# Optimization experiments

Hardware: AMD Instinct MI355X
Metric: run time of the kernel (lower is better)

The kernel has to match this reference:

```python
import jax, jax.numpy as jnp
import numpy as np

B, T, C, J = 2048, 128, 3, 25   # batch, frames, coords, joints
E = 64                          # structure elements (n_elements)


def setup_inputs() -> dict:
    key = jax.random.key(0)
    k1, k2 = jax.random.split(key)
    x = jax.random.normal(k1, (B, T, C, J), dtype=jnp.float32)
    centres = jax.random.uniform(k2, (E, 2), dtype=jnp.float32)
    sharpness = jnp.full((E, 2), 3.0, dtype=jnp.float32)  # torch init: ones*3
    return {"x": x, "centres": centres, "sharpness": sharpness}


def _mst_deaths(Dm):
    """Prim's MST over dense distance matrix Dm [n,n].
    The multiset of MST edge weights equals the finite death times of the
    0-dim Vietoris-Rips persistence diagram (births are all 0)."""
    n = Dm.shape[0]
    in_tree0 = jnp.zeros(n, dtype=bool).at[0].set(True)

    def step(carry, _):
        mind, in_tree = carry
        masked = jnp.where(in_tree, jnp.inf, mind)  # distance from tree to each node
        j = jnp.argmin(masked)
        w = masked[j]                               # weight of edge added to MST
        in_tree = in_tree.at[j].set(True)
        mind = jnp.minimum(mind, Dm[j])
        return (mind, in_tree), w

    (_, _), deaths = jax.lax.scan(step, (Dm[0], in_tree0), None, length=n - 1)
    return deaths  # [n-1]


def reference(x, centres, sharpness):
    # --- dense preprocessing ---
    h = x.mean(1)                           # [B, C, J]
    h = h[..., :, None] - h[..., None, :]   # [B, C, J, J] pairwise coord diffs
    h = h.mean(-3)                          # [B, J, J]
    h = jnp.sqrt((h * h).sum(axis=1))       # torch.norm(., 2, dim=1) -> [B, J]
    lo, hi = h.min(), h.max()
    rng = hi - lo
    safe = rng > 1e-8
    h = jnp.where(safe, (h - lo) / jnp.where(safe, rng, 1.0), jnp.zeros_like(h))

    # --- Vietoris-Rips dim-0 persistence on point cloud h: B points in J dims ---
    sq = (h * h).sum(-1)
    d2 = sq[:, None] + sq[None, :] - 2.0 * (h @ h.T)       # [B, B]
    Dm = jnp.sqrt(jnp.maximum(d2, 1e-12))
    deaths = _mst_deaths(Dm)                               # [B-1]
    pd = jnp.stack([jnp.zeros_like(deaths), deaths], -1)[None]  # [1, P, 2]

    # --- StructureElementLayer: out[b,e] = sum_p exp(-sum_d s[e,d]^2 (pd-c)^2) ---
    s2 = sharpness * sharpness                             # [E, 2]
    diff = pd[:, :, None, :] - centres[None, None, :, :]   # [1, P, E, 2]
    out = jnp.exp(-(diff * diff * s2).sum(-1)).sum(1)      # [1, E]
    return out
```

## Files before the change

### kernel.cpp

```cpp
#include <hip/hip_runtime.h>
#include <math.h>

#define B_N 2048
#define T_N 128
#define C_N 3
#define J_N 25
#define E_N 64
#define TC  (T_N*C_N)
#define TCJ (TC*J_N)
#define NQ4 (TCJ/4)
#define NC  128

#define D_OFF      0
#define H_OFF      (B_N*B_N)
#define BLO_OFF    (H_OFF + B_N*J_N)
#define BHI_OFF    (BLO_OFF + B_N)
#define DEATHS_OFF (BHI_OFF + B_N)
#define BEST_OFF   (DEATHS_OFF + B_N)
#define COMP_OFF   (BEST_OFF + 4*B_N)
#define GC_OFF     (COMP_OFF + 2*B_N)
#define DC_OFF     (GC_OFF + 2)

typedef unsigned long long u64;
#define U64MAX 0xFFFFFFFFFFFFFFFFull
#define U32INF 0xFFFFFFFFu

__global__ void __launch_bounds__(256) k_reduce(const float* __restrict__ x,
                                                float* __restrict__ ws) {
    __shared__ float4 part[250];
    __shared__ float S[100];
    __shared__ float Mj[25];
    const int t = threadIdx.x, b = blockIdx.x;
    const float4* x4 = (const float4*)(x + (size_t)b * TCJ);
    if (t < 250) {
        float4 a; a.x = a.y = a.z = a.w = 0.f;
        for (int idx = t; idx < NQ4; idx += 250) {
            float4 v = x4[idx];
            a.x += v.x; a.y += v.y; a.z += v.z; a.w += v.w;
        }
        part[t] = a;
    }
    __syncthreads();
    if (t < 25) {
        float4 s = part[t];
        #pragma unroll
        for (int g = 1; g < 10; ++g) {
            float4 v = part[t + 25 * g];
            s.x += v.x; s.y += v.y; s.z += v.z; s.w += v.w;
        }
        S[4*t] = s.x; S[4*t+1] = s.y; S[4*t+2] = s.z; S[4*t+3] = s.w;
    }
    __syncthreads();
    if (t < 25) Mj[t] = (S[t] + S[t+25] + S[t+50] + S[t+75]) * (1.0f / 384.0f);
    __syncthreads();
    if (t < 25) {
        float mj = Mj[t], acc = 0.f;
        #pragma unroll
        for (int i = 0; i < J_N; ++i) { float d = Mj[i] - mj; acc += d * d; }
        float hv = sqrtf(acc);
        ws[H_OFF + b * J_N + t] = hv;
        S[t] = hv;
    }
    __syncthreads();
    if (t == 0) {
        float lo = S[0], hi = S[0];
        #pragma unroll
        for (int i = 1; i < J_N; ++i) { lo = fminf(lo, S[i]); hi = fmaxf(hi, S[i]); }
        ws[BLO_OFF + b] = lo;
        ws[BHI_OFF + b] = hi;
    }
}

__global__ void __launch_bounds__(1024) k_distscan(float* __restrict__ ws) {
    __shared__ float A[16][26];
    __shared__ float Bsh[1024 * J_N];
    const int t = threadIdx.x, blk = blockIdx.x;
    const int ty = t >> 6, tx = t & 63;
    const float* h = ws + H_OFF;
    const int row0 = blk * 16;
    for (int idx = t; idx < 16 * J_N; idx += 1024)
        A[idx / J_N][idx % J_N] = h[(row0 + idx / J_N) * J_N + idx % J_N];
    if (blk < 16) ((unsigned*)(ws + DC_OFF))[blk * 1024 + t] = U32INF;
    if (blk == 0) {
        unsigned* gc = (unsigned*)(ws + COMP_OFF);
        gc[t] = (unsigned)t; gc[t + 1024] = (unsigned)(t + 1024);
        if (t == 0) { ((unsigned*)(ws + GC_OFF))[0] = 0u; ((unsigned*)(ws + GC_OFF))[1] = 0u; }
    }
    const int row = row0 + ty;
    float ar[J_N];
    u64 bestk = U64MAX;
    float* D = ws + D_OFF;
    for (int mt = 0; mt < 2; ++mt) {
        __syncthreads();
        for (int idx = t; idx < 1024 * J_N; idx += 1024)
            Bsh[idx] = h[mt * 1024 * J_N + idx];
        __syncthreads();
        if (mt == 0) {
            #pragma unroll
            for (int k = 0; k < J_N; ++k) ar[k] = A[ty][k];
        }
        #pragma unroll 4
        for (int cc = 0; cc < 16; ++cc) {
            const int col = mt * 1024 + cc * 64 + tx;
            const float* bp = &Bsh[(cc * 64 + tx) * J_N];
            float acc = 0.f;
            #pragma unroll
            for (int k = 0; k < J_N; ++k) { float d = ar[k] - bp[k]; acc += d * d; }
            float dist = sqrtf(fmaxf(acc, 1e-12f));
            D[(size_t)row * B_N + col] = dist;
            if (col != row) {
                unsigned a = min((unsigned)row, (unsigned)col);
                unsigned b2 = max((unsigned)row, (unsigned)col);
                u64 key = ((u64)__float_as_uint(dist) << 32) | (a << 11) | b2;
                if (key < bestk) bestk = key;
            }
        }
    }
    #pragma unroll
    for (int off = 32; off; off >>= 1) {
        u64 o = __shfl_down(bestk, off);
        if (o < bestk) bestk = o;
    }
    if (tx == 0) ((u64*)(ws + BEST_OFF))[row] = bestk;
}

__global__ void __launch_bounds__(1024) k_round(float* __restrict__ ws, int par_in) {
    unsigned* gcnt = (unsigned*)(ws + GC_OFF);
    const unsigned base = gcnt[par_in];
    if (base >= B_N - 1) return;
    __shared__ __align__(16) unsigned comp[B_N];
    __shared__ u64 cb[B_N];
    __shared__ unsigned par[B_N];
    __shared__ unsigned cnt_s;
    const int t = threadIdx.x, blk = blockIdx.x;
    const unsigned* gcomp_in = (const unsigned*)(ws + COMP_OFF) + par_in * B_N;
    unsigned* gcomp_out = (unsigned*)(ws + COMP_OFF) + (par_in ^ 1) * B_N;
    const u64* bin = (const u64*)(ws + BEST_OFF) + par_in * B_N;
    u64* bout = (u64*)(ws + BEST_OFF) + (par_in ^ 1) * B_N;
    float* deaths = ws + DEATHS_OFF;

    if (t == 0) cnt_s = 0u;
    comp[t] = gcomp_in[t]; comp[t + 1024] = gcomp_in[t + 1024];
    cb[t] = U64MAX; cb[t + 1024] = U64MAX;
    __syncthreads();
    #pragma unroll
    for (int i = t; i < B_N; i += 1024) {
        u64 bk = bin[i];
        if (bk != U64MAX) atomicMin(&cb[comp[i]], bk);
    }
    __syncthreads();
    #pragma unroll
    for (int c = t; c < B_N; c += 1024) {
        u64 k = cb[c];
        unsigned p = (unsigned)c;
        if (k != U64MAX) {
            unsigned a  = (unsigned)((k >> 11) & 0x7FFu);
            unsigned b2 = (unsigned)(k & 0x7FFu);
            unsigned ca = comp[a], cbv = comp[b2];
            unsigned c2 = (ca == (unsigned)c) ? cbv : ca;
            p = c2;
            if (!(cb[c2] == k && c2 < (unsigned)c)) {
                unsigned li = atomicAdd(&cnt_s, 1u);
                if (blk == 0) deaths[base + li] = __uint_as_float((unsigned)(k >> 32));
            }
        }
        par[c] = p;
    }
    __syncthreads();
    #pragma unroll
    for (int c = t; c < B_N; c += 1024) {
        unsigned p = par[c];
        if (p != (unsigned)c && par[p] == (unsigned)c && (unsigned)c < p) par[c] = (unsigned)c;
    }
    __syncthreads();
    #pragma unroll
    for (int c = t; c < B_N; c += 1024) {
        unsigned r = par[c];
        while (true) { unsigned pr = par[r]; if (pr == r) break; r = pr; }
        par[c] = r;
    }
    __syncthreads();
    #pragma unroll
    for (int i = t; i < B_N; i += 1024) comp[i] = par[comp[i]];
    __syncthreads();
    const unsigned newbase = base + cnt_s;
    if (blk == 0) {
        gcomp_out[t] = comp[t]; gcomp_out[t + 1024] = comp[t + 1024];
        if (t == 0) { gcnt[par_in ^ 1] = newbase; if (newbase >= B_N - 1) gcnt[par_in] = newbase; }
    }
    if (newbase >= B_N - 1) return;

    const int w = t >> 6, lane = t & 63;
    const int row = blk * 16 + w;
    const unsigned ci = comp[row];
    u64 prev = bin[row];
    {
        unsigned pa = (unsigned)((prev >> 11) & 0x7FFu);
        unsigned pb = (unsigned)(prev & 0x7FFu);
        unsigned jo = (pa == (unsigned)row) ? pb : pa;
        if (comp[jo] != ci) {
            if (lane == 0) bout[row] = prev;
            return;
        }
    }
    const float4* row4 = (const float4*)(ws + D_OFF + (size_t)row * B_N);
    const uint4* comp4 = (const uint4*)comp;
    u64 best = U64MAX;
    #pragma unroll
    for (int k = 0; k < 8; ++k) {
        const int q = k * 64 + lane;
        float4 w4 = row4[q];
        uint4  c4 = comp4[q];
        const unsigned j0 = (unsigned)(q * 4);
        float wv[4] = {w4.x, w4.y, w4.z, w4.w};
        unsigned cv[4] = {c4.x, c4.y, c4.z, c4.w};
        #pragma unroll
        for (int m = 0; m < 4; ++m) {
            if (cv[m] != ci) {
                unsigned j = j0 + m;
                unsigned a = min((unsigned)row, j), b2 = max((unsigned)row, j);
                u64 key = ((u64)__float_as_uint(wv[m]) << 32) | (a << 11) | b2;
                if (key < best) best = key;
            }
        }
    }
    #pragma unroll
    for (int off = 32; off; off >>= 1) {
        u64 o = __shfl_down(best, off);
        if (o < best) best = o;
    }
    if (lane == 0) bout[row] = best;
}

__global__ void __launch_bounds__(1024) k_round4c(float* __restrict__ ws) {
    unsigned* gcnt = (unsigned*)(ws + GC_OFF);
    const unsigned base = gcnt[1];
    if (base >= B_N - 1) return;
    __shared__ __align__(16) unsigned comp[B_N];
    __shared__ __align__(16) unsigned ovl[NC*NC];
    __shared__ unsigned cflag[B_N];
    __shared__ unsigned cnt_s, csum[16];
    u64* cb = (u64*)ovl;
    unsigned* par = ovl + 4096;
    const int t = threadIdx.x, blk = blockIdx.x;
    const unsigned* gcomp_in = (const unsigned*)(ws + COMP_OFF) + B_N;
    const u64* bin = (const u64*)(ws + BEST_OFF) + B_N;
    float* deaths = ws + DEATHS_OFF;

    if (t == 0) cnt_s = 0u;
    comp[t] = gcomp_in[t]; comp[t + 1024] = gcomp_in[t + 1024];
    cb[t] = U64MAX; cb[t + 1024] = U64MAX;
    __syncthreads();
    #pragma unroll
    for (int i = t; i < B_N; i += 1024) {
        u64 bk = bin[i];
        if (bk != U64MAX) atomicMin(&cb[comp[i]], bk);
    }
    __syncthreads();
    #pragma unroll
    for (int c = t; c < B_N; c += 1024) {
        u64 k = cb[c];
        unsigned p = (unsigned)c;
        if (k != U64MAX) {
            unsigned a  = (unsigned)((k >> 11) & 0x7FFu);
            unsigned b2 = (unsigned)(k & 0x7FFu);
            unsigned ca = comp[a], cbv = comp[b2];
            unsigned c2 = (ca == (unsigned)c) ? cbv : ca;
            p = c2;
            if (!(cb[c2] == k && c2 < (unsigned)c)) {
                unsigned li = atomicAdd(&cnt_s, 1u);
                if (blk == 0) deaths[base + li] = __uint_as_float((unsigned)(k >> 32));
            }
        }
        par[c] = p;
    }
    __syncthreads();
    #pragma unroll
    for (int c = t; c < B_N; c += 1024) {
        unsigned p = par[c];
        if (p != (unsigned)c && par[p] == (unsigned)c && (unsigned)c < p) par[c] = (unsigned)c;
    }
    __syncthreads();
    #pragma unroll
    for (int c = t; c < B_N; c += 1024) {
        unsigned r = par[c];
        while (true) { unsigned pr = par[r]; if (pr == r) break; r = pr; }
        par[c] = r;
    }
    __syncthreads();
    #pragma unroll
    for (int i = t; i < B_N; i += 1024) comp[i] = par[comp[i]];
    __syncthreads();
    const unsigned newbase = base + cnt_s;
    if (blk == 0 && t == 0) { gcnt[0] = newbase; gcnt[1] = newbase; }
    if (newbase >= B_N - 1) return;

    cflag[t] = 0u; cflag[t + 1024] = 0u;
    __syncthreads();
    cflag[comp[t]] = 1u; cflag[comp[t + 1024]] = 1u;
    __syncthreads();
    const unsigned lane = t & 63, w = t >> 6;
    unsigned f0 = cflag[2 * t], f1 = cflag[2 * t + 1];
    unsigned s = f0 + f1, sc = s;
    #pragma unroll
    for (int off = 1; off < 64; off <<= 1) {
        unsigned v = __shfl_up(sc, off);
        if (lane >= (unsigned)off) sc += v;
    }
    if (lane == 63) csum[w] = sc;
    __syncthreads();
    if (t < 16) {
        unsigned v = csum[t], acc = v;
        #pragma unroll
        for (int off = 1; off < 16; off <<= 1) {
            unsigned u2 = __shfl_up(acc, off);
            if (t >= off) acc += u2;
        }
        csum[t] = acc - v;
    }
    __syncthreads();
    unsigned off0 = csum[w] + (sc - s);
    __syncthreads();
    if (f0) cflag[2 * t] = off0;
    if (f1) cflag[2 * t + 1] = off0 + f0;
    __syncthreads();

    #pragma unroll
    for (int i = 0; i < 16; ++i) ovl[i * 1024 + t] = U32INF;
    __syncthreads();
    {
        const int row = blk * 16 + (int)w;
        const unsigned ci = comp[row];
        const unsigned ri = cflag[ci];
        const float4* row4 = (const float4*)(ws + D_OFF + (size_t)row * B_N);
        const uint4* comp4 = (const uint4*)comp;
        #pragma unroll
        for (int k = 0; k < 8; ++k) {
            const int q = k * 64 + (int)lane;
            float4 w4 = row4[q];
            uint4  c4 = comp4[q];
            float wv[4] = {w4.x, w4.y, w4.z, w4.w};
            unsigned cv[4] = {c4.x, c4.y, c4.z, c4.w};
            #pragma unroll
            for (int m = 0; m < 4; ++m) {
                if (cv[m] != ci) atomicMin(&ovl[ri * NC + cflag[cv[m]]], __float_as_uint(wv[m]));
            }
        }
    }
    __syncthreads();
    unsigned* gDc = (unsigned*)(ws + DC_OFF);
    #pragma unroll
    for (int i = t; i < NC * NC; i += 1024) {
        unsigned v = ovl[i];
        if (v != U32INF) atomicMin(&gDc[i], v);
    }
}

__global__ void __launch_bounds__(1024) k_finishstruct(float* __restrict__ ws,
                                                       const float* __restrict__ centres,
                                                       const float* __restrict__ sharp,
                                                       float* __restrict__ out) {
    __shared__ unsigned Dcs[NC * NC];
    __shared__ u64 cbf[NC];
    __shared__ unsigned parf[NC], ccomp[NC];
    __shared__ unsigned cnt_s, base_s;
    __shared__ float redlo[16], redhi[16];
    const int t = threadIdx.x;
    const int lane = t & 63, w = t >> 6;
    float* deaths = ws + DEATHS_OFF;
    const unsigned base0 = ((const unsigned*)(ws + GC_OFF))[0];

    if (base0 < B_N - 1) {
        const unsigned* gDc = (const unsigned*)(ws + DC_OFF);
        #pragma unroll
        for (int i = 0; i < 16; ++i) Dcs[i * 1024 + t] = gDc[i * 1024 + t];
        if (t < NC) ccomp[t] = (unsigned)t;
        if (t == 0) base_s = base0;
        __syncthreads();
        for (int iter = 0; iter < 7; ++iter) {
            if (t < NC) cbf[t] = U64MAX;
            if (t == 0) cnt_s = 0u;
            __syncthreads();
            #pragma unroll
            for (int q = 0; q < 8; ++q) {
                const int r = w * 8 + q;
                const unsigned cc = ccomp[r];
                u64 key = U64MAX;
                #pragma unroll
                for (int hh = 0; hh < 2; ++hh) {
                    const int c = lane + hh * 64;
                    unsigned wv = Dcs[r * NC + c];
                    if (wv != U32INF && ccomp[c] != cc) {
                        unsigned a = min((unsigned)r, (unsigned)c);
                        unsigned b2 = max((unsigned)r, (unsigned)c);
                        u64 k2 = ((u64)wv << 32) | (a << 7) | b2;
                        if (k2 < key) key = k2;
                    }
                }
                #pragma unroll
                for (int off = 32; off; off >>= 1) {
                    u64 o = __shfl_down(key, off);
                    if (o < key) key = o;
                }
                if (lane == 0 && key != U64MAX) atomicMin(&cbf[cc], key);
            }
            __syncthreads();
            bool add = false; float dw = 0.f;
            if (t < NC) {
                u64 k = cbf[t];
                unsigned p = (unsigned)t;
                if (k != U64MAX) {
                    unsigned a = (unsigned)((k >> 7) & 127u), b2 = (unsigned)(k & 127u);
                    unsigned ca = ccomp[a], cbv = ccomp[b2];
                    unsigned c2 = (ca == (unsigned)t) ? cbv : ca;
                    p = c2;
                    if (!(cbf[c2] == k && c2 < (unsigned)t)) {
                        add = true; dw = __uint_as_float((unsigned)(k >> 32));
                    }
                }
                parf[t] = p;
            }
            __syncthreads();
            if (t < NC) {
                unsigned pp = parf[t];
                if (pp != (unsigned)t && parf[pp] == (unsigned)t && (unsigned)t < pp) parf[t] = (unsigned)t;
            }
            __syncthreads();
            if (t < NC) {
                unsigned r2 = parf[t];
                while (parf[r2] != r2) r2 = parf[r2];
                parf[t] = r2;
            }
            __syncthreads();
            if (t < NC) {
                if (add) { unsigned li = atomicAdd(&cnt_s, 1u); deaths[base_s + li] = dw; }
                ccomp[t] = parf[ccomp[t]];
            }
            __syncthreads();
            if (t == 0) base_s += cnt_s;
            __syncthreads();
            if (base_s >= B_N - 1) break;
        }
        __threadfence_block();
        __syncthreads();
    }

    float lo = INFINITY, hi = -INFINITY;
    #pragma unroll
    for (int i = t; i < B_N; i += 1024) {
        lo = fminf(lo, ws[BLO_OFF + i]);
        hi = fmaxf(hi, ws[BHI_OFF + i]);
    }
    #pragma unroll
    for (int off = 32; off; off >>= 1) {
        lo = fminf(lo, __shfl_down(lo, off));
        hi = fmaxf(hi, __shfl_down(hi, off));
    }
    if (lane == 0) { redlo[w] = lo; redhi[w] = hi; }
    __syncthreads();
    lo = redlo[0]; hi = redhi[0];
    #pragma unroll
    for (int k = 1; k < 16; ++k) { lo = fminf(lo, redlo[k]); hi = fmaxf(hi, redhi[k]); }
    float rng = hi - lo;
    float rinv = (rng > 1e-8f) ? 1.0f / rng : 0.0f;

    for (int e = w; e < E_N; e += 16) {
        const float c0 = centres[e * 2], c1 = centres[e * 2 + 1];
        const float s0 = sharp[e * 2],   s1 = sharp[e * 2 + 1];
        const float s1sq = s1 * s1;
        float acc = 0.f;
        for (int p = lane; p < B_N - 1; p += 64) {
            float d = deaths[p] * rinv - c1;
            acc += expf(-s1sq * d * d);
        }
        #pragma unroll
        for (int off = 32; off; off >>= 1) acc += __shfl_down(acc, off);
        if (lane == 0) out[e] = expf(-s0 * s0 * c0 * c0) * acc;
    }
}

extern "C" void kernel_launch(void* const* d_in, const int* in_sizes, int n_in,
                              void* d_out, int out_size, void* d_ws, size_t ws_size,
                              hipStream_t stream) {
    const float* x       = (const float*)d_in[0];
    const float* centres = (const float*)d_in[1];
    const float* sharp   = (const float*)d_in[2];
    float* out = (float*)d_out;
    float* ws  = (float*)d_ws;

    hipLaunchKernelGGL(k_reduce,   dim3(B_N),  dim3(256),  0, stream, x, ws);
    hipLaunchKernelGGL(k_distscan, dim3(128),  dim3(1024), 0, stream, ws);
    hipLaunchKernelGGL(k_round,    dim3(128),  dim3(1024), 0, stream, ws, 0);
    hipLaunchKernelGGL(k_round,    dim3(128),  dim3(1024), 0, stream, ws, 1);
    hipLaunchKernelGGL(k_round,    dim3(128),  dim3(1024), 0, stream, ws, 0);
    hipLaunchKernelGGL(k_round4c,  dim3(128),  dim3(1024), 0, stream, ws);
    hipLaunchKernelGGL(k_finishstruct, dim3(1), dim3(1024), 0, stream, ws, centres, sharp, out);
}
```

Measured before the change: 183.4 us.

## Contract graph one Borůvka round earlier and store finish-stage weights as 16-bit

Removes the fourth Borůvka round kernel and builds the contracted component graph after three rounds, now sized for up to 256 components instead of 128. To fit the 256×256 component distance matrix in shared memory in the single-block finish kernel, weights are truncated to their upper 16 bits, which is bfloat16-like precision. The contraction kernel now keeps one per-row partial in shared memory and flushes it with global atomicMin, instead of accumulating a full matrix per block. The intent is to save one launch and one full pass over the distance matrix. In exchange, the serial single-block finish stage does more work, there are more global atomics, and the reduced weight precision can change death values and tie ordering.

```diff
diff --git a/kernel.cpp b/kernel.cpp
--- a/kernel.cpp
+++ b/kernel.cpp
@@ -9,7 +9,7 @@
 #define TC  (T_N*C_N)
 #define TCJ (TC*J_N)
 #define NQ4 (TCJ/4)
-#define NC  128
+#define NC  256
 
 #define D_OFF      0
 #define H_OFF      (B_N*B_N)
@@ -80,7 +80,7 @@
     const int row0 = blk * 16;
     for (int idx = t; idx < 16 * J_N; idx += 1024)
         A[idx / J_N][idx % J_N] = h[(row0 + idx / J_N) * J_N + idx % J_N];
-    if (blk < 16) ((unsigned*)(ws + DC_OFF))[blk * 1024 + t] = U32INF;
+    if (blk < 64) ((unsigned*)(ws + DC_OFF))[blk * 1024 + t] = U32INF;
     if (blk == 0) {
         unsigned* gc = (unsigned*)(ws + COMP_OFF);
         gc[t] = (unsigned)t; gc[t + 1024] = (unsigned)(t + 1024);
@@ -232,19 +232,19 @@
     if (lane == 0) bout[row] = best;
 }
 
-__global__ void __launch_bounds__(1024) k_round4c(float* __restrict__ ws) {
+__global__ void __launch_bounds__(1024) k_round3c(float* __restrict__ ws) {
     unsigned* gcnt = (unsigned*)(ws + GC_OFF);
-    const unsigned base = gcnt[1];
+    const unsigned base = gcnt[0];
     if (base >= B_N - 1) return;
     __shared__ __align__(16) unsigned comp[B_N];
-    __shared__ __align__(16) unsigned ovl[NC*NC];
+    __shared__ u64 cb[B_N];
+    __shared__ unsigned par[B_N];
     __shared__ unsigned cflag[B_N];
+    __shared__ unsigned pd[16][NC];
     __shared__ unsigned cnt_s, csum[16];
-    u64* cb = (u64*)ovl;
-    unsigned* par = ovl + 4096;
     const int t = threadIdx.x, blk = blockIdx.x;
-    const unsigned* gcomp_in = (const unsigned*)(ws + COMP_OFF) + B_N;
-    const u64* bin = (const u64*)(ws + BEST_OFF) + B_N;
+    const unsigned* gcomp_in = (const unsigned*)(ws + COMP_OFF);
+    const u64* bin = (const u64*)(ws + BEST_OFF);
     float* deaths = ws + DEATHS_OFF;
 
     if (t == 0) cnt_s = 0u;
@@ -326,12 +326,11 @@
     __syncthreads();
 
     #pragma unroll
-    for (int i = 0; i < 16; ++i) ovl[i * 1024 + t] = U32INF;
-    __syncthreads();
+    for (int i = 0; i < 4; ++i) pd[0][i * 1024 + t] = U32INF;
+    __syncthreads();
+    const int row = blk * 16 + (int)w;
+    const unsigned ci = comp[row];
     {
-        const int row = blk * 16 + (int)w;
-        const unsigned ci = comp[row];
-        const unsigned ri = cflag[ci];
         const float4* row4 = (const float4*)(ws + D_OFF + (size_t)row * B_N);
         const uint4* comp4 = (const uint4*)comp;
         #pragma unroll
@@ -343,16 +342,16 @@
             unsigned cv[4] = {c4.x, c4.y, c4.z, c4.w};
             #pragma unroll
             for (int m = 0; m < 4; ++m) {
-                if (cv[m] != ci) atomicMin(&ovl[ri * NC + cflag[cv[m]]], __float_as_uint(wv[m]));
+                if (cv[m] != ci) atomicMin(&pd[w][cflag[cv[m]]], __float_as_uint(wv[m]));
             }
         }
     }
     __syncthreads();
     unsigned* gDc = (unsigned*)(ws + DC_OFF);
-    #pragma unroll
-    for (int i = t; i < NC * NC; i += 1024) {
-        unsigned v = ovl[i];
-        if (v != U32INF) atomicMin(&gDc[i], v);
+    const unsigned ri = cflag[ci];
+    for (int j2 = (int)lane; j2 < NC; j2 += 64) {
+        unsigned v = pd[w][j2];
+        if (v != U32INF) atomicMin(&gDc[ri * NC + j2], v);
     }
 }
 
@@ -360,7 +359,7 @@
                                                        const float* __restrict__ centres,
                                                        const float* __restrict__ sharp,
                                                        float* __restrict__ out) {
-    __shared__ unsigned Dcs[NC * NC];
+    __shared__ unsigned short Dcs[NC * NC];
     __shared__ u64 cbf[NC];
     __shared__ unsigned parf[NC], ccomp[NC];
     __shared__ unsigned cnt_s, base_s;
@@ -373,27 +372,30 @@
     if (base0 < B_N - 1) {
         const unsigned* gDc = (const unsigned*)(ws + DC_OFF);
         #pragma unroll
-        for (int i = 0; i < 16; ++i) Dcs[i * 1024 + t] = gDc[i * 1024 + t];
+        for (int i = 0; i < 64; ++i) {
+            unsigned v = gDc[i * 1024 + t];
+            Dcs[i * 1024 + t] = (unsigned short)(v >> 16);
+        }
         if (t < NC) ccomp[t] = (unsigned)t;
         if (t == 0) base_s = base0;
         __syncthreads();
-        for (int iter = 0; iter < 7; ++iter) {
+        for (int iter = 0; iter < 8; ++iter) {
             if (t < NC) cbf[t] = U64MAX;
             if (t == 0) cnt_s = 0u;
             __syncthreads();
             #pragma unroll
-            for (int q = 0; q < 8; ++q) {
-                const int r = w * 8 + q;
+            for (int q = 0; q < 16; ++q) {
+                const int r = w * 16 + q;
                 const unsigned cc = ccomp[r];
                 u64 key = U64MAX;
                 #pragma unroll
-                for (int hh = 0; hh < 2; ++hh) {
+                for (int hh = 0; hh < 4; ++hh) {
                     const int c = lane + hh * 64;
                     unsigned wv = Dcs[r * NC + c];
-                    if (wv != U32INF && ccomp[c] != cc) {
+                    if (wv != 0xFFFFu && ccomp[c] != cc) {
                         unsigned a = min((unsigned)r, (unsigned)c);
                         unsigned b2 = max((unsigned)r, (unsigned)c);
-                        u64 k2 = ((u64)wv << 32) | (a << 7) | b2;
+                        u64 k2 = ((u64)wv << 32) | (a << 8) | b2;
                         if (k2 < key) key = k2;
                     }
                 }
@@ -410,12 +412,13 @@
                 u64 k = cbf[t];
                 unsigned p = (unsigned)t;
                 if (k != U64MAX) {
-                    unsigned a = (unsigned)((k >> 7) & 127u), b2 = (unsigned)(k & 127u);
+                    unsigned a = (unsigned)((k >> 8) & 255u), b2 = (unsigned)(k & 255u);
                     unsigned ca = ccomp[a], cbv = ccomp[b2];
                     unsigned c2 = (ca == (unsigned)t) ? cbv : ca;
                     p = c2;
                     if (!(cbf[c2] == k && c2 < (unsigned)t)) {
-                        add = true; dw = __uint_as_float((unsigned)(k >> 32));
+                        add = true;
+                        dw = __uint_as_float((unsigned)(k >> 32) << 16);
                     }
                 }
                 parf[t] = p;
@@ -441,7 +444,6 @@
             __syncthreads();
             if (base_s >= B_N - 1) break;
         }
-        __threadfence_block();
         __syncthreads();
     }
 
@@ -492,7 +494,6 @@
     hipLaunchKernelGGL(k_distscan, dim3(128),  dim3(1024), 0, stream, ws);
     hipLaunchKernelGGL(k_round,    dim3(128),  dim3(1024), 0, stream, ws, 0);
     hipLaunchKernelGGL(k_round,    dim3(128),  dim3(1024), 0, stream, ws, 1);
-    hipLaunchKernelGGL(k_round,    dim3(128),  dim3(1024), 0, stream, ws, 0);
-    hipLaunchKernelGGL(k_round4c,  dim3(128),  dim3(1024), 0, stream, ws);
+    hipLaunchKernelGGL(k_round3c,  dim3(128),  dim3(1024), 0, stream, ws);
     hipLaunchKernelGGL(k_finishstruct, dim3(1), dim3(1024), 0, stream, ws, centres, sharp, out);
 }
```

After: 178.8 us. 1.03x faster.
